# Kernel optimization log

Measured on AMD Instinct MI355X. Metric: run time of the kernel, lower is better.

Reference implementation:

```python
import jax, jax.numpy as jnp
import numpy as np

UNITS = 512
IN_DIM = 256


def setup_inputs() -> dict:
    key = jax.random.key(0)
    k1, k2, k3 = jax.random.split(key, 3)
    x = jax.random.normal(k1, (128, 512, IN_DIM), dtype=jnp.float32)
    # glorot_uniform for kernel
    lim = float(np.sqrt(6.0 / (IN_DIM + UNITS)))
    kernel = jax.random.uniform(k2, (IN_DIM, UNITS), minval=-lim, maxval=lim, dtype=jnp.float32)
    # orthogonal init for recurrent kernel
    a = jax.random.normal(k3, (UNITS, UNITS), dtype=jnp.float32)
    q, r = jnp.linalg.qr(a)
    recurrent_kernel = q * jnp.sign(jnp.diag(r))[None, :]
    bias = jnp.zeros((UNITS,), dtype=jnp.float32)
    return {"x": x, "kernel": kernel, "recurrent_kernel": recurrent_kernel, "bias": bias}


def reference(x, kernel, recurrent_kernel, bias):
    # h_t = tanh(x_t @ W_x + b + h_{t-1} @ W_h), return full sequence [B, T, U]
    B = x.shape[0]
    # Precompute input projection for all timesteps in one batched GEMM
    xp = jnp.einsum('btf,fu->btu', x, kernel) + bias  # [B, T, U]

    def step(h, xp_t):
        h_new = jnp.tanh(xp_t + h @ recurrent_kernel)
        return h_new, h_new

    h0 = jnp.zeros((B, UNITS), dtype=x.dtype)
    _, ys = jax.lax.scan(step, h0, jnp.swapaxes(xp, 0, 1))  # ys: [T, B, U]
    return jnp.swapaxes(ys, 0, 1)
```

## Files before the change

kernel.cpp:

```cpp
#include <hip/hip_runtime.h>
#include <math.h>


#define BM 64
#define BN 64
#define BK 32
#define SENT 0xFFFFFFFFu

__global__ __launch_bounds__(256) void xp_gemm(
    const float* __restrict__ x,
    const float* __restrict__ wx,
    const float* __restrict__ bias,
    float* __restrict__ xp)
{
    __shared__ float As[BK][BM + 4];
    __shared__ float Bs[BK][BN + 4];

    const int tid = threadIdx.x;
    const int m0 = blockIdx.y * BM;
    const int n0 = blockIdx.x * BN;
    const int tm = tid / 16;
    const int tn = tid % 16;

    float acc[4][4] = {};

    for (int k0 = 0; k0 < 256; k0 += BK) {
        {
            const int kk = tid % BK;
            const int r0 = tid / BK;
            #pragma unroll
            for (int rr = 0; rr < 8; ++rr) {
                const int m = r0 + rr * 8;
                As[kk][m] = x[(size_t)(m0 + m) * 256 + (k0 + kk)];
            }
        }
        {
            const int nn = tid % BN;
            const int r0 = tid / BN;
            #pragma unroll
            for (int rr = 0; rr < 8; ++rr) {
                const int k = r0 + rr * 4;
                Bs[k][nn] = wx[(size_t)(k0 + k) * 512 + (n0 + nn)];
            }
        }
        __syncthreads();

        #pragma unroll
        for (int kk = 0; kk < BK; ++kk) {
            const float4 a = *(const float4*)&As[kk][tm * 4];
            const float4 b = *(const float4*)&Bs[kk][tn * 4];
            const float av[4] = {a.x, a.y, a.z, a.w};
            const float bv[4] = {b.x, b.y, b.z, b.w};
            #pragma unroll
            for (int i = 0; i < 4; ++i)
                #pragma unroll
                for (int j = 0; j < 4; ++j)
                    acc[i][j] += av[i] * bv[j];
        }
        __syncthreads();
    }

    #pragma unroll
    for (int i = 0; i < 4; ++i) {
        const int m = m0 + tm * 4 + i;
        #pragma unroll
        for (int j = 0; j < 4; ++j) {
            const int n = n0 + tn * 4 + j;
            xp[(size_t)m * 512 + n] = acc[i][j] + bias[n];
        }
    }
}

#define FMA4(A, W, H) { (A).x += (H)*(W).x; (A).y += (H)*(W).y; (A).z += (H)*(W).z; (A).w += (H)*(W).w; }

__global__ __launch_bounds__(1024) void rnn_scan4(
    const float* __restrict__ wh,
    const float* __restrict__ xp,
    float* __restrict__ out)
{
    __shared__ float h_lds[2][512];
    __shared__ float red[32][2][128];

    const int tid = threadIdx.x;
    const int us  = blockIdx.x & 3;
    const int bg  = blockIdx.x >> 2;
    const int u0  = us * 128;
    const int g   = tid & 31;
    const int s   = tid >> 5;
    const int kbase = s * 16;
    const size_t seq = 512 * 512;

    const float* wr = &wh[(size_t)kbase * 512 + (u0 + 4 * g)];
    const float4 w0  = *(const float4*)(wr + 0  * 512);
    const float4 w1  = *(const float4*)(wr + 1  * 512);
    const float4 w2  = *(const float4*)(wr + 2  * 512);
    const float4 w3  = *(const float4*)(wr + 3  * 512);
    const float4 w4  = *(const float4*)(wr + 4  * 512);
    const float4 w5  = *(const float4*)(wr + 5  * 512);
    const float4 w6  = *(const float4*)(wr + 6  * 512);
    const float4 w7  = *(const float4*)(wr + 7  * 512);
    const float4 w8  = *(const float4*)(wr + 8  * 512);
    const float4 w9  = *(const float4*)(wr + 9  * 512);
    const float4 w10 = *(const float4*)(wr + 10 * 512);
    const float4 w11 = *(const float4*)(wr + 11 * 512);
    const float4 w12 = *(const float4*)(wr + 12 * 512);
    const float4 w13 = *(const float4*)(wr + 13 * 512);
    const float4 w14 = *(const float4*)(wr + 14 * 512);
    const float4 w15 = *(const float4*)(wr + 15 * 512);

    const int ru = tid & 127;
    const int rb = (tid >> 7) & 1;
    const float* xpp = xp + (size_t)(bg * 2 + rb) * seq + u0 + ru;
    float*       hop = out + (size_t)(bg * 2 + rb) * seq + u0 + ru;

    const int sb   = (tid >= 384) ? 1 : 0;
    const int srem = tid - sb * 384;
    const int shk  = (srem < u0) ? srem : srem + 128;
    const float* pollp = out + (size_t)(bg * 2 + sb) * seq + shk;

    for (int t = 0; t < 512; ++t) {
        float xpv = 0.0f;
        if (tid < 256) xpv = xpp[(size_t)t * 512];

        if (t == 0) {
            ((float*)h_lds)[tid] = 0.0f;
        } else if (tid < 768) {
            const float* p = pollp + (size_t)(t - 1) * 512;
            float v;
            int cnt = 0;
            do {
                v = __hip_atomic_load(p, __ATOMIC_RELAXED, __HIP_MEMORY_SCOPE_AGENT);
                if (__float_as_uint(v) != SENT) break;
                __builtin_amdgcn_s_sleep(1);
            } while (++cnt < (1 << 20));
            h_lds[sb][shk] = v;
        }
        __syncthreads();

        float4 a0 = make_float4(0.f, 0.f, 0.f, 0.f);
        float4 a1 = make_float4(0.f, 0.f, 0.f, 0.f);
        const float* hb0 = &h_lds[0][kbase];
        const float* hb1 = &h_lds[1][kbase];
        #define STEP4(W0, W1, W2, W3, OFF) { \
            const float4 h0 = *(const float4*)(hb0 + (OFF)); \
            const float4 h1 = *(const float4*)(hb1 + (OFF)); \
            FMA4(a0, W0, h0.x) FMA4(a0, W1, h0.y) FMA4(a0, W2, h0.z) FMA4(a0, W3, h0.w) \
            FMA4(a1, W0, h1.x) FMA4(a1, W1, h1.y) FMA4(a1, W2, h1.z) FMA4(a1, W3, h1.w) }
        STEP4(w0,  w1,  w2,  w3,  0)
        STEP4(w4,  w5,  w6,  w7,  4)
        STEP4(w8,  w9,  w10, w11, 8)
        STEP4(w12, w13, w14, w15, 12)
        #undef STEP4

        *(float4*)&red[s][0][4 * g] = a0;
        *(float4*)&red[s][1][4 * g] = a1;
        __syncthreads();

        if (tid < 256) {
            float r = xpv;
            #pragma unroll
            for (int ss = 0; ss < 32; ++ss) r += red[ss][rb][ru];
            const float hn = tanhf(r);
            h_lds[rb][u0 + ru] = hn;
            __hip_atomic_store(hop + (size_t)t * 512, hn,
                               __ATOMIC_RELAXED, __HIP_MEMORY_SCOPE_AGENT);
        }
        __syncthreads();
    }
}

__global__ __launch_bounds__(1024) void rnn_scan3(
    const float* __restrict__ wh, float* __restrict__ out, int* __restrict__ flags)
{
    __shared__ float smem[21504];
    float* h_lds = smem;
    float* red   = smem + 1024;

    const int tid = threadIdx.x;
    const int us  = blockIdx.x & 3;
    const int bg  = blockIdx.x >> 2;
    const int u0  = us * 128;
    const int g   = tid & 31;
    const int s   = tid >> 5;
    const int kbase = s * 16;

    float4 w[16];
    #pragma unroll
    for (int i = 0; i < 16; ++i)
        w[i] = *(const float4*)&wh[(size_t)(kbase + i) * 512 + (u0 + 4 * g)];

    float* out0 = out + (size_t)(bg * 2 + 0) * (512 * 512);
    float* out1 = out + (size_t)(bg * 2 + 1) * (512 * 512);
    const int ru = tid & 127;
    const int rb = tid >> 7;
    int* myflag = flags + bg * 512;

    for (int t = 0; t < 512; ++t) {
        float xpv = 0.f;
        if (tid < 256) {
            const float* op = (rb == 0) ? out0 : out1;
            xpv = op[(size_t)t * 512 + u0 + ru];
        }
        if (t == 0) {
            h_lds[tid] = 0.f;
        } else {
            if (tid == 0) {
                int v, cnt = 0;
                do {
                    v = __hip_atomic_load(&myflag[t - 1], __ATOMIC_RELAXED, __HIP_MEMORY_SCOPE_AGENT);
                    if (v < 4) __builtin_amdgcn_s_sleep(2);
                } while (v < 4 && ++cnt < (1 << 22));
                (void)__hip_atomic_load(&myflag[t - 1], __ATOMIC_ACQUIRE, __HIP_MEMORY_SCOPE_AGENT);
            }
            __syncthreads();
            const int hb = tid >> 9;
            const int hk = tid & 511;
            const float* src = ((hb == 0) ? out0 : out1) + (size_t)(t - 1) * 512 + hk;
            h_lds[hb * 512 + hk] = __hip_atomic_load(src, __ATOMIC_RELAXED, __HIP_MEMORY_SCOPE_AGENT);
        }
        __syncthreads();

        float4 a0 = make_float4(0.f, 0.f, 0.f, 0.f);
        float4 a1 = make_float4(0.f, 0.f, 0.f, 0.f);
        #pragma unroll
        for (int i = 0; i < 4; ++i) {
            const float4 h0 = *(const float4*)&h_lds[0 * 512 + kbase + 4 * i];
            const float4 h1 = *(const float4*)&h_lds[1 * 512 + kbase + 4 * i];
            FMA4(a0, w[4*i+0], h0.x) FMA4(a0, w[4*i+1], h0.y) FMA4(a0, w[4*i+2], h0.z) FMA4(a0, w[4*i+3], h0.w)
            FMA4(a1, w[4*i+0], h1.x) FMA4(a1, w[4*i+1], h1.y) FMA4(a1, w[4*i+2], h1.z) FMA4(a1, w[4*i+3], h1.w)
        }
        *(float4*)&red[(s * 2 + 0) * 128 + 4 * g] = a0;
        *(float4*)&red[(s * 2 + 1) * 128 + 4 * g] = a1;
        __syncthreads();

        if (tid < 256) {
            float r = xpv;
            #pragma unroll
            for (int ss = 0; ss < 32; ++ss) r += red[(ss * 2 + rb) * 128 + ru];
            const float hn = tanhf(r);
            float* op = (rb == 0) ? out0 : out1;
            __hip_atomic_store(&op[(size_t)t * 512 + u0 + ru], hn,
                               __ATOMIC_RELAXED, __HIP_MEMORY_SCOPE_AGENT);
        }
        __syncthreads();
        if (tid == 0)
            __hip_atomic_fetch_add(&myflag[t], 1, __ATOMIC_RELEASE, __HIP_MEMORY_SCOPE_AGENT);
    }
}

__global__ __launch_bounds__(1024, 4) void rnn_scan2(
    const float* __restrict__ wh, float* __restrict__ out)
{
    __shared__ float h_lds[2][512];
    __shared__ float red[8][2][512];

    const int tid = threadIdx.x;
    const int g = tid & 127;
    const int s = tid >> 7;
    const int b = tid >> 9;
    const int u = tid & 511;

    float* seqb = out + (size_t)(2 * blockIdx.x + b) * 512 * 512;
    h_lds[b][u] = 0.0f;
    __syncthreads();

    const float4* __restrict__ whv = (const float4*)wh;
    const int kbase = s * 64;

    for (int t = 0; t < 512; ++t) {
        const float xpv = seqb[(size_t)t * 512 + u];
        float4 a0 = make_float4(0.f, 0.f, 0.f, 0.f);
        float4 a1 = make_float4(0.f, 0.f, 0.f, 0.f);
        #pragma unroll 4
        for (int kk = 0; kk < 64; kk += 4) {
            const int k = kbase + kk;
            const float4 h0 = *(const float4*)&h_lds[0][k];
            const float4 h1 = *(const float4*)&h_lds[1][k];
            const float4 v0 = whv[(k + 0) * 128 + g];
            const float4 v1 = whv[(k + 1) * 128 + g];
            const float4 v2 = whv[(k + 2) * 128 + g];
            const float4 v3 = whv[(k + 3) * 128 + g];
            FMA4(a0, v0, h0.x) FMA4(a0, v1, h0.y) FMA4(a0, v2, h0.z) FMA4(a0, v3, h0.w)
            FMA4(a1, v0, h1.x) FMA4(a1, v1, h1.y) FMA4(a1, v2, h1.z) FMA4(a1, v3, h1.w)
        }
        *(float4*)&red[s][0][4 * g] = a0;
        *(float4*)&red[s][1][4 * g] = a1;
        __syncthreads();
        float r = xpv;
        #pragma unroll
        for (int ss = 0; ss < 8; ++ss) r += red[ss][b][u];
        const float hn = tanhf(r);
        h_lds[b][u] = hn;
        seqb[(size_t)t * 512 + u] = hn;
        __syncthreads();
    }
}

extern "C" void kernel_launch(void* const* d_in, const int* in_sizes, int n_in,
                              void* d_out, int out_size, void* d_ws, size_t ws_size,
                              hipStream_t stream) {
    const float* x    = (const float*)d_in[0];
    const float* wx   = (const float*)d_in[1];
    const float* wh   = (const float*)d_in[2];
    const float* bias = (const float*)d_in[3];
    float* out = (float*)d_out;

    dim3 g1(512 / BN, 65536 / BM);
    const size_t xp_bytes = (size_t)128 * 512 * 512 * sizeof(float);
    const size_t flag_bytes = 64 * 512 * sizeof(int);

    if (d_ws != nullptr && ws_size >= xp_bytes) {
        hipMemsetAsync(d_out, 0xFF, xp_bytes, stream);
        xp_gemm<<<g1, 256, 0, stream>>>(x, wx, bias, (float*)d_ws);
        rnn_scan4<<<256, 1024, 0, stream>>>(wh, (const float*)d_ws, out);
    } else if (d_ws != nullptr && ws_size >= flag_bytes) {
        hipMemsetAsync(d_ws, 0, flag_bytes, stream);
        xp_gemm<<<g1, 256, 0, stream>>>(x, wx, bias, out);
        rnn_scan3<<<256, 1024, 0, stream>>>(wh, out, (int*)d_ws);
    } else {
        xp_gemm<<<g1, 256, 0, stream>>>(x, wx, bias, out);
        rnn_scan2<<<64, 1024, 0, stream>>>(wh, out);
    }
}
```

Baseline: 1.225 ms.

## Fuse sentinel fill into GEMM, remap scan blocks, drop trailing barrier

The separate memset of the output to a sentinel value is removed, and each GEMM tile now writes the sentinel into its own output region, which saves one full pass over memory. The scan kernel remaps block indices so the four unit slices of a batch group are spread across the grid instead of sitting next to each other. Polling now spins tightly for a few tries before sleeping, and the per-step trailing __syncthreads is removed. Dropping that barrier relies on the h_lds double buffering and the later barriers for correctness, which is a race risk. The unused flag-based scan variant is also deleted.

```diff
diff --git a/kernel.cpp b/kernel.cpp
--- a/kernel.cpp
+++ b/kernel.cpp
@@ -2,51 +2,57 @@
 #include <math.h>
 
 
-#define BM 64
-#define BN 64
-#define BK 32
 #define SENT 0xFFFFFFFFu
-
-__global__ __launch_bounds__(256) void xp_gemm(
+#define ALF(p)    __hip_atomic_load((p), __ATOMIC_RELAXED, __HIP_MEMORY_SCOPE_AGENT)
+#define ASF(p, v) __hip_atomic_store((p), (v), __ATOMIC_RELAXED, __HIP_MEMORY_SCOPE_AGENT)
+#define FMA4(A, W, H) { (A).x += (H)*(W).x; (A).y += (H)*(W).y; (A).z += (H)*(W).z; (A).w += (H)*(W).w; }
+
+__global__ __launch_bounds__(256) void xp_gemm_sent(
     const float* __restrict__ x,
     const float* __restrict__ wx,
     const float* __restrict__ bias,
-    float* __restrict__ xp)
-{
-    __shared__ float As[BK][BM + 4];
-    __shared__ float Bs[BK][BN + 4];
-
-    const int tid = threadIdx.x;
-    const int m0 = blockIdx.y * BM;
-    const int n0 = blockIdx.x * BN;
+    float* __restrict__ xp,
+    float* __restrict__ out)
+{
+    __shared__ float As[32][68];
+    __shared__ float Bs[32][68];
+
+    const int tid = threadIdx.x;
+    const int m0 = blockIdx.y * 64;
+    const int n0 = blockIdx.x * 64;
     const int tm = tid / 16;
     const int tn = tid % 16;
 
+    {
+        const float s = __uint_as_float(SENT);
+        const float4 sv = make_float4(s, s, s, s);
+        const int r = tid >> 4;
+        const int c = (tid & 15) * 4;
+        float* op = out + (size_t)m0 * 512 + n0;
+        #pragma unroll
+        for (int i = 0; i < 4; ++i)
+            *(float4*)&op[(size_t)(r + 16 * i) * 512 + c] = sv;
+    }
+
     float acc[4][4] = {};
 
-    for (int k0 = 0; k0 < 256; k0 += BK) {
-        {
-            const int kk = tid % BK;
-            const int r0 = tid / BK;
-            #pragma unroll
-            for (int rr = 0; rr < 8; ++rr) {
-                const int m = r0 + rr * 8;
-                As[kk][m] = x[(size_t)(m0 + m) * 256 + (k0 + kk)];
-            }
-        }
-        {
-            const int nn = tid % BN;
-            const int r0 = tid / BN;
-            #pragma unroll
-            for (int rr = 0; rr < 8; ++rr) {
-                const int k = r0 + rr * 4;
-                Bs[k][nn] = wx[(size_t)(k0 + k) * 512 + (n0 + nn)];
-            }
-        }
-        __syncthreads();
-
-        #pragma unroll
-        for (int kk = 0; kk < BK; ++kk) {
+    for (int k0 = 0; k0 < 256; k0 += 32) {
+        {
+            const int kk = tid % 32, r0 = tid / 32;
+            #pragma unroll
+            for (int rr = 0; rr < 8; ++rr)
+                As[kk][r0 + rr * 8] = x[(size_t)(m0 + r0 + rr * 8) * 256 + (k0 + kk)];
+        }
+        {
+            const int nn = tid % 64, r0 = tid / 64;
+            #pragma unroll
+            for (int rr = 0; rr < 8; ++rr)
+                Bs[r0 + rr * 4][nn] = wx[(size_t)(k0 + r0 + rr * 4) * 512 + (n0 + nn)];
+        }
+        __syncthreads();
+
+        #pragma unroll
+        for (int kk = 0; kk < 32; ++kk) {
             const float4 a = *(const float4*)&As[kk][tm * 4];
             const float4 b = *(const float4*)&Bs[kk][tn * 4];
             const float av[4] = {a.x, a.y, a.z, a.w};
@@ -61,19 +67,14 @@
     }
 
     #pragma unroll
-    for (int i = 0; i < 4; ++i) {
-        const int m = m0 + tm * 4 + i;
-        #pragma unroll
-        for (int j = 0; j < 4; ++j) {
-            const int n = n0 + tn * 4 + j;
-            xp[(size_t)m * 512 + n] = acc[i][j] + bias[n];
-        }
-    }
-}
-
-#define FMA4(A, W, H) { (A).x += (H)*(W).x; (A).y += (H)*(W).y; (A).z += (H)*(W).z; (A).w += (H)*(W).w; }
-
-__global__ __launch_bounds__(1024) void rnn_scan4(
+    for (int i = 0; i < 4; ++i)
+        #pragma unroll
+        for (int j = 0; j < 4; ++j)
+            xp[(size_t)(m0 + tm * 4 + i) * 512 + (n0 + tn * 4 + j)] =
+                acc[i][j] + bias[n0 + tn * 4 + j];
+}
+
+__global__ __launch_bounds__(1024) void rnn_scan9(
     const float* __restrict__ wh,
     const float* __restrict__ xp,
     float* __restrict__ out)
@@ -82,8 +83,8 @@
     __shared__ float red[32][2][128];
 
     const int tid = threadIdx.x;
-    const int us  = blockIdx.x & 3;
-    const int bg  = blockIdx.x >> 2;
+    const int us  = blockIdx.x >> 6;
+    const int bg  = blockIdx.x & 63;
     const int u0  = us * 128;
     const int g   = tid & 31;
     const int s   = tid >> 5;
@@ -126,13 +127,12 @@
             ((float*)h_lds)[tid] = 0.0f;
         } else if (tid < 768) {
             const float* p = pollp + (size_t)(t - 1) * 512;
-            float v;
-            int cnt = 0;
-            do {
-                v = __hip_atomic_load(p, __ATOMIC_RELAXED, __HIP_MEMORY_SCOPE_AGENT);
-                if (__float_as_uint(v) != SENT) break;
-                __builtin_amdgcn_s_sleep(1);
-            } while (++cnt < (1 << 20));
+            float v = ALF(p);
+            int it = 0;
+            while (__float_as_uint(v) == SENT && ++it < (1 << 22)) {
+                if (it > 32) __builtin_amdgcn_s_sleep(1);
+                v = ALF(p);
+            }
             h_lds[sb][shk] = v;
         }
         __syncthreads();
@@ -161,91 +161,58 @@
             #pragma unroll
             for (int ss = 0; ss < 32; ++ss) r += red[ss][rb][ru];
             const float hn = tanhf(r);
+            ASF(hop + (size_t)t * 512, hn);
             h_lds[rb][u0 + ru] = hn;
-            __hip_atomic_store(hop + (size_t)t * 512, hn,
-                               __ATOMIC_RELAXED, __HIP_MEMORY_SCOPE_AGENT);
-        }
-        __syncthreads();
-    }
-}
-
-__global__ __launch_bounds__(1024) void rnn_scan3(
-    const float* __restrict__ wh, float* __restrict__ out, int* __restrict__ flags)
-{
-    __shared__ float smem[21504];
-    float* h_lds = smem;
-    float* red   = smem + 1024;
-
-    const int tid = threadIdx.x;
-    const int us  = blockIdx.x & 3;
-    const int bg  = blockIdx.x >> 2;
-    const int u0  = us * 128;
-    const int g   = tid & 31;
-    const int s   = tid >> 5;
-    const int kbase = s * 16;
-
-    float4 w[16];
+        }
+    }
+}
+
+__global__ __launch_bounds__(256) void xp_gemm_plain(
+    const float* __restrict__ x, const float* __restrict__ wx,
+    const float* __restrict__ bias, float* __restrict__ xp)
+{
+    __shared__ float As[32][68];
+    __shared__ float Bs[32][68];
+    const int tid = threadIdx.x;
+    const int m0 = blockIdx.y * 64;
+    const int n0 = blockIdx.x * 64;
+    const int tm = tid / 16;
+    const int tn = tid % 16;
+    float acc[4][4] = {};
+    for (int k0 = 0; k0 < 256; k0 += 32) {
+        {
+            const int kk = tid % 32, r0 = tid / 32;
+            #pragma unroll
+            for (int rr = 0; rr < 8; ++rr)
+                As[kk][r0 + rr * 8] = x[(size_t)(m0 + r0 + rr * 8) * 256 + (k0 + kk)];
+        }
+        {
+            const int nn = tid % 64, r0 = tid / 64;
+            #pragma unroll
+            for (int rr = 0; rr < 8; ++rr)
+                Bs[r0 + rr * 4][nn] = wx[(size_t)(k0 + r0 + rr * 4) * 512 + (n0 + nn)];
+        }
+        __syncthreads();
+        #pragma unroll
+        for (int kk = 0; kk < 32; ++kk) {
+            const float4 a = *(const float4*)&As[kk][tm * 4];
+            const float4 b = *(const float4*)&Bs[kk][tn * 4];
+            const float av[4] = {a.x, a.y, a.z, a.w};
+            const float bv[4] = {b.x, b.y, b.z, b.w};
+            #pragma unroll
+            for (int i = 0; i < 4; ++i)
+                #pragma unroll
+                for (int j = 0; j < 4; ++j)
+                    acc[i][j] += av[i] * bv[j];
+        }
+        __syncthreads();
+    }
     #pragma unroll
-    for (int i = 0; i < 16; ++i)
-        w[i] = *(const float4*)&wh[(size_t)(kbase + i) * 512 + (u0 + 4 * g)];
-
-    float* out0 = out + (size_t)(bg * 2 + 0) * (512 * 512);
-    float* out1 = out + (size_t)(bg * 2 + 1) * (512 * 512);
-    const int ru = tid & 127;
-    const int rb = tid >> 7;
-    int* myflag = flags + bg * 512;
-
-    for (int t = 0; t < 512; ++t) {
-        float xpv = 0.f;
-        if (tid < 256) {
-            const float* op = (rb == 0) ? out0 : out1;
-            xpv = op[(size_t)t * 512 + u0 + ru];
-        }
-        if (t == 0) {
-            h_lds[tid] = 0.f;
-        } else {
-            if (tid == 0) {
-                int v, cnt = 0;
-                do {
-                    v = __hip_atomic_load(&myflag[t - 1], __ATOMIC_RELAXED, __HIP_MEMORY_SCOPE_AGENT);
-                    if (v < 4) __builtin_amdgcn_s_sleep(2);
-                } while (v < 4 && ++cnt < (1 << 22));
-                (void)__hip_atomic_load(&myflag[t - 1], __ATOMIC_ACQUIRE, __HIP_MEMORY_SCOPE_AGENT);
-            }
-            __syncthreads();
-            const int hb = tid >> 9;
-            const int hk = tid & 511;
-            const float* src = ((hb == 0) ? out0 : out1) + (size_t)(t - 1) * 512 + hk;
-            h_lds[hb * 512 + hk] = __hip_atomic_load(src, __ATOMIC_RELAXED, __HIP_MEMORY_SCOPE_AGENT);
-        }
-        __syncthreads();
-
-        float4 a0 = make_float4(0.f, 0.f, 0.f, 0.f);
-        float4 a1 = make_float4(0.f, 0.f, 0.f, 0.f);
-        #pragma unroll
-        for (int i = 0; i < 4; ++i) {
-            const float4 h0 = *(const float4*)&h_lds[0 * 512 + kbase + 4 * i];
-            const float4 h1 = *(const float4*)&h_lds[1 * 512 + kbase + 4 * i];
-            FMA4(a0, w[4*i+0], h0.x) FMA4(a0, w[4*i+1], h0.y) FMA4(a0, w[4*i+2], h0.z) FMA4(a0, w[4*i+3], h0.w)
-            FMA4(a1, w[4*i+0], h1.x) FMA4(a1, w[4*i+1], h1.y) FMA4(a1, w[4*i+2], h1.z) FMA4(a1, w[4*i+3], h1.w)
-        }
-        *(float4*)&red[(s * 2 + 0) * 128 + 4 * g] = a0;
-        *(float4*)&red[(s * 2 + 1) * 128 + 4 * g] = a1;
-        __syncthreads();
-
-        if (tid < 256) {
-            float r = xpv;
-            #pragma unroll
-            for (int ss = 0; ss < 32; ++ss) r += red[(ss * 2 + rb) * 128 + ru];
-            const float hn = tanhf(r);
-            float* op = (rb == 0) ? out0 : out1;
-            __hip_atomic_store(&op[(size_t)t * 512 + u0 + ru], hn,
-                               __ATOMIC_RELAXED, __HIP_MEMORY_SCOPE_AGENT);
-        }
-        __syncthreads();
-        if (tid == 0)
-            __hip_atomic_fetch_add(&myflag[t], 1, __ATOMIC_RELEASE, __HIP_MEMORY_SCOPE_AGENT);
-    }
+    for (int i = 0; i < 4; ++i)
+        #pragma unroll
+        for (int j = 0; j < 4; ++j)
+            xp[(size_t)(m0 + tm * 4 + i) * 512 + (n0 + tn * 4 + j)] =
+                acc[i][j] + bias[n0 + tn * 4 + j];
 }
 
 __global__ __launch_bounds__(1024, 4) void rnn_scan2(
@@ -253,20 +220,16 @@
 {
     __shared__ float h_lds[2][512];
     __shared__ float red[8][2][512];
-
     const int tid = threadIdx.x;
     const int g = tid & 127;
     const int s = tid >> 7;
     const int b = tid >> 9;
     const int u = tid & 511;
-
     float* seqb = out + (size_t)(2 * blockIdx.x + b) * 512 * 512;
     h_lds[b][u] = 0.0f;
     __syncthreads();
-
     const float4* __restrict__ whv = (const float4*)wh;
     const int kbase = s * 64;
-
     for (int t = 0; t < 512; ++t) {
         const float xpv = seqb[(size_t)t * 512 + u];
         float4 a0 = make_float4(0.f, 0.f, 0.f, 0.f);
@@ -305,20 +268,14 @@
     const float* bias = (const float*)d_in[3];
     float* out = (float*)d_out;
 
-    dim3 g1(512 / BN, 65536 / BM);
     const size_t xp_bytes = (size_t)128 * 512 * 512 * sizeof(float);
-    const size_t flag_bytes = 64 * 512 * sizeof(int);
+    dim3 g1(512 / 64, 65536 / 64);
 
     if (d_ws != nullptr && ws_size >= xp_bytes) {
-        hipMemsetAsync(d_out, 0xFF, xp_bytes, stream);
-        xp_gemm<<<g1, 256, 0, stream>>>(x, wx, bias, (float*)d_ws);
-        rnn_scan4<<<256, 1024, 0, stream>>>(wh, (const float*)d_ws, out);
-    } else if (d_ws != nullptr && ws_size >= flag_bytes) {
-        hipMemsetAsync(d_ws, 0, flag_bytes, stream);
-        xp_gemm<<<g1, 256, 0, stream>>>(x, wx, bias, out);
-        rnn_scan3<<<256, 1024, 0, stream>>>(wh, out, (int*)d_ws);
+        xp_gemm_sent<<<g1, 256, 0, stream>>>(x, wx, bias, (float*)d_ws, out);
+        rnn_scan9<<<256, 1024, 0, stream>>>(wh, (const float*)d_ws, out);
     } else {
-        xp_gemm<<<g1, 256, 0, stream>>>(x, wx, bias, out);
+        xp_gemm_plain<<<g1, 256, 0, stream>>>(x, wx, bias, out);
         rnn_scan2<<<64, 1024, 0, stream>>>(wh, out);
     }
 }
```

Measured after the change: 1.290 ms. 5.4% more time.
